# Performance work log

Measured on AMD Instinct MI355X. Metric: run time of the kernel, lower is better.

Reference implementation:

```python
import jax, jax.numpy as jnp
import numpy as np

NUM_HEADS = 16
HEAD_DIM = 64
HIDDEN = NUM_HEADS * HEAD_DIM  # 1024
SEQ_LEN = 4096


def setup_inputs() -> dict:
    key = jax.random.key(0)
    ks = jax.random.split(key, 8)
    hidden_states = jax.random.normal(ks[0], (SEQ_LEN, HIDDEN), dtype=jnp.float32)
    cu_seqlens = jnp.sort(jax.random.randint(ks[1], (5,), 0, SEQ_LEN)).astype(jnp.int32)
    cos = jax.random.uniform(ks[2], (SEQ_LEN, HEAD_DIM), dtype=jnp.float32)
    sin = jax.random.uniform(ks[3], (SEQ_LEN, HEAD_DIM), dtype=jnp.float32)
    W_qkv = jax.random.normal(ks[4], (HIDDEN, 3 * HIDDEN), dtype=jnp.float32) * 0.02
    b_qkv = jax.random.normal(ks[5], (3 * HIDDEN,), dtype=jnp.float32) * 0.02
    W_proj = jax.random.normal(ks[6], (HIDDEN, HIDDEN), dtype=jnp.float32) * 0.02
    b_proj = jax.random.normal(ks[7], (HIDDEN,), dtype=jnp.float32) * 0.02
    return {
        "hidden_states": hidden_states,
        "cu_seqlens": cu_seqlens,
        "cos": cos,
        "sin": sin,
        "W_qkv": W_qkv,
        "b_qkv": b_qkv,
        "W_proj": W_proj,
        "b_proj": b_proj,
    }


def _rotate_half(x):
    x1, x2 = jnp.split(x, 2, axis=-1)
    return jnp.concatenate([-x2, x1], axis=-1)


def reference(hidden_states, cu_seqlens, cos, sin, W_qkv, b_qkv, W_proj, b_proj):
    # NOTE: original module does not use cu_seqlens for masking (full dense attention).
    seq_len = hidden_states.shape[0]
    qkv = hidden_states @ W_qkv + b_qkv  # (S, 3*H)
    qkv = qkv.reshape(seq_len, 3, NUM_HEADS, HEAD_DIM)
    q, k, v = qkv[:, 0], qkv[:, 1], qkv[:, 2]  # (S, nh, hd)
    c = cos[:, None, :]
    s = sin[:, None, :]
    q = q * c + _rotate_half(q) * s
    k = k * c + _rotate_half(k) * s
    scale = 1.0 / jnp.sqrt(jnp.float32(HEAD_DIM))
    # (nh, S, hd)
    q = q.transpose(1, 0, 2)
    k = k.transpose(1, 0, 2)
    v = v.transpose(1, 0, 2)
    attn = jnp.einsum('hqd,hkd->hqk', q, k) * scale
    attn = jax.nn.softmax(attn, axis=-1)
    out = jnp.einsum('hqk,hkd->hqd', attn, v)
    out = out.transpose(1, 0, 2).reshape(seq_len, HIDDEN)
    return out @ W_proj + b_proj
```

## Files before the change

### kernel.cpp

```cpp
#include <hip/hip_runtime.h>
#include <type_traits>

typedef short bf16x8 __attribute__((ext_vector_type(8)));
typedef float f32x4  __attribute__((ext_vector_type(4)));
typedef unsigned short u16;

#define MFMA(a,b,c) __builtin_amdgcn_mfma_f32_16x16x32_bf16((a),(b),(c),0,0,0)

__device__ __forceinline__ float bf2f(u16 u){ unsigned x=((unsigned)u)<<16; return __builtin_bit_cast(float,x); }
__device__ __forceinline__ u16 f2bf(float f){ unsigned x=__builtin_bit_cast(unsigned,f); x += 0x7fffu + ((x>>16)&1u); return (u16)(x>>16); }

#if __has_builtin(__builtin_amdgcn_cvt_pk_bf16_f32)
typedef __bf16 hwbf2 __attribute__((ext_vector_type(2)));
__device__ __forceinline__ unsigned pkbf(float a, float b){
  hwbf2 r = __builtin_amdgcn_cvt_pk_bf16_f32(a, b);
  return __builtin_bit_cast(unsigned, r);
}
#else
__device__ __forceinline__ unsigned pkbf(float a, float b){
  unsigned ua = __builtin_bit_cast(unsigned, a), ub = __builtin_bit_cast(unsigned, b);
  ua += 0x7fffu + ((ua>>16)&1u);
  ub += 0x7fffu + ((ub>>16)&1u);
  return __builtin_amdgcn_perm(ub, ua, 0x07060302u);
}
#endif

#if __has_builtin(__builtin_amdgcn_exp2f)
#define EXP2(x) __builtin_amdgcn_exp2f(x)
#else
#define EXP2(x) exp2f(x)
#endif

__device__ __forceinline__ void async_cp16(const u16* g, u16* l){
  __builtin_amdgcn_global_load_lds((const __attribute__((address_space(1))) void*)g,
                                   (__attribute__((address_space(3))) void*)l, 16, 0, 0);
}

__global__ __launch_bounds__(256) void prep(
    const float* __restrict__ H, const float* __restrict__ Wqkv, const float* __restrict__ Wproj,
    u16* __restrict__ Hb, u16* __restrict__ WqkvT, u16* __restrict__ WprojT)
{
  __shared__ u16 tile[32][33];
  const int bid = blockIdx.x, tid = threadIdx.x;
  if (bid < 4096) {
    int i = (bid*256 + tid)*4;
    float4 v = *(const float4*)(H + i);
    ushort4 o;
    o.x = f2bf(v.x); o.y = f2bf(v.y); o.z = f2bf(v.z); o.w = f2bf(v.w);
    *(ushort4*)(Hb + i) = o;
    return;
  }
  const float* in; u16* out; int R, C, bx, by;
  if (bid < 7168) { int t = bid-4096; in=Wqkv; out=WqkvT; R=1024; C=3072; bx=t%96; by=t/96; }
  else            { int t = bid-7168; in=Wproj; out=WprojT; R=1024; C=1024; bx=t%32; by=t/32; }
  int bc = bx*32, br = by*32;
  int tx = tid & 31, ty = tid >> 5;
  #pragma unroll
  for (int i=ty;i<32;i+=8) tile[i][tx] = f2bf(in[(size_t)(br+i)*C + bc + tx]);
  __syncthreads();
  #pragma unroll
  for (int i=ty;i<32;i+=8) out[(size_t)(bc+i)*R + br + tx] = tile[tx][i];
}

__global__ __launch_bounds__(256) void gemm_qkv_rope(
    const u16* __restrict__ A, const u16* __restrict__ Bt,
    const float* __restrict__ bias, const float* __restrict__ cosb, const float* __restrict__ sinb,
    u16* __restrict__ Qo, u16* __restrict__ Ko, u16* __restrict__ Vo)
{
  constexpr int K = 1024;
  __shared__ __align__(16) u16 As[128*64];
  __shared__ __align__(16) u16 Bs[128*64];
  const int m0 = blockIdx.y*128, n0 = blockIdx.x*128;
  const int tid = threadIdx.x, wave = tid>>6, lane = tid&63;
  const int wr = (wave>>1)*64, wc = (wave&1)*64;
  const int ml = lane&15, quad = lane>>4;
  const int lrow8 = lane>>3, lchk = lane&7;
  const int swzg = (lchk ^ lrow8)*8;
  const u16* gA[4]; u16* lA[4];
  const u16* gB[4]; u16* lB[4];
  #pragma unroll
  for (int t=0;t<4;t++){
    gA[t] = A  + (size_t)(m0 + wave*32 + t*8 + lrow8)*K + swzg;
    lA[t] = &As[(wave*32 + t*8)*64];
    gB[t] = Bt + (size_t)(n0 + wave*32 + t*8 + lrow8)*K + swzg;
    lB[t] = &Bs[(wave*32 + t*8)*64];
  }
  f32x4 acc[4][4] = {};
  const int rch0 = ( quad     ^ (ml&7))*8;
  const int rch1 = ((quad|4) ^ (ml&7))*8;
  for (int k0=0; k0<K; k0+=64) {
    #pragma unroll
    for (int t=0;t<4;t++){ async_cp16(gA[t]+k0, lA[t]); async_cp16(gB[t]+k0, lB[t]); }
    __syncthreads();
    #pragma unroll
    for (int kk=0;kk<2;kk++){
      const int rc = kk ? rch1 : rch0;
      bf16x8 af[4], bfr[4];
      #pragma unroll
      for (int i=0;i<4;i++)  af[i]  = *(const bf16x8*)&As[(wr+i*16+ml)*64 + rc];
      #pragma unroll
      for (int j=0;j<4;j++) bfr[j] = *(const bf16x8*)&Bs[(wc+j*16+ml)*64 + rc];
      #pragma unroll
      for (int i=0;i<4;i++)
        #pragma unroll
        for (int j=0;j<4;j++)
          acc[i][j] = MFMA(af[i], bfr[j], acc[i][j]);
    }
    __syncthreads();
  }
  const int region = n0 >> 10;
  if (region == 2) {
    #pragma unroll
    for (int j=0;j<4;j++){
      int col = n0 + wc + j*16 + ml;
      int dloc = col & 63, hh = (col & 1023) >> 6;
      float bv = bias[col];
      #pragma unroll
      for (int i=0;i<4;i++){
        int row0 = m0 + wr + i*16 + quad*4;
        #pragma unroll
        for (int r=0;r<4;r++)
          Vo[((size_t)hh*4096 + row0 + r)*64 + dloc] = f2bf(acc[i][j][r] + bv);
      }
    }
  } else {
    u16* dst = region ? Ko : Qo;
    const float qs = region ? 1.0f : 0.125f*1.44269504f;
    #pragma unroll
    for (int j=0;j<4;j++){
      int col = n0 + wc + j*16 + ml;
      int dloc = col & 63, hh = (col & 1023) >> 6;
      float bv  = bias[col];
      float bvp = bias[col ^ 32];
      float sgn = (dloc < 32) ? -1.f : 1.f;
      #pragma unroll
      for (int i=0;i<4;i++){
        int row0 = m0 + wr + i*16 + quad*4;
        #pragma unroll
        for (int r=0;r<4;r++){
          int t = row0 + r;
          float c = cosb[t*64 + dloc], s = sinb[t*64 + dloc];
          float val = acc[i][j][r]   + bv;
          float par = acc[i][j^2][r] + bvp;
          dst[((size_t)hh*4096 + t)*64 + dloc] = f2bf((val*c + sgn*par*s)*qs);
        }
      }
    }
  }
}

__global__ __launch_bounds__(256) void vtrans_perm_bf16(const u16* __restrict__ in, u16* __restrict__ out){
  __shared__ u16 tile[32][33];
  const int h = blockIdx.z;
  const u16* ip = in + (size_t)h*4096*64;
  u16* op = out + (size_t)h*64*4096;
  int bt = blockIdx.x*32, bd = blockIdx.y*32;
  int tx = threadIdx.x & 31, ty = threadIdx.x >> 5;
  #pragma unroll
  for (int i=ty;i<32;i+=8) tile[i][tx] = ip[(size_t)(bt+i)*64 + bd + tx];
  __syncthreads();
  const int tlog = ((tx>>2)&1)*16 + (tx>>3)*4 + (tx&3);
  #pragma unroll
  for (int i=ty;i<32;i+=8) op[(size_t)(bd+i)*4096 + bt + tx] = tile[tlog][i];
}

template<int BN, typename OutT>
__global__ __launch_bounds__(256) void gemm_bt_bias(
    const u16* __restrict__ A, const u16* __restrict__ Bt,
    const float* __restrict__ bias, OutT* __restrict__ C,
    int M, int N, int K)
{
  __shared__ __align__(16) u16 As[128*64];
  __shared__ __align__(16) u16 Bs[BN*64];
  const int m0 = blockIdx.y*128, n0 = blockIdx.x*BN;
  const int tid = threadIdx.x, wave = tid>>6, lane = tid&63;
  const int wr = (wave>>1)*64, wc = (wave&1)*(BN/2);
  const int ml = lane&15, quad = lane>>4;
  const int lrow8 = lane>>3, lchk = lane&7;
  const int swzg = (lchk ^ lrow8)*8;
  const u16* gA[4]; u16* lA[4];
  #pragma unroll
  for (int t=0;t<4;t++){
    gA[t] = A + (size_t)(m0 + wave*32 + t*8 + lrow8)*K + swzg;
    lA[t] = &As[(wave*32 + t*8)*64];
  }
  constexpr int BI = BN/32;
  const u16* gB[BI]; u16* lB[BI];
  #pragma unroll
  for (int t=0;t<BI;t++){
    gB[t] = Bt + (size_t)(n0 + wave*(BN/4) + t*8 + lrow8)*K + swzg;
    lB[t] = &Bs[(wave*(BN/4) + t*8)*64];
  }
  constexpr int NJ = BN/32;
  f32x4 acc[4][NJ] = {};
  const int rch0 = ( quad     ^ (ml&7))*8;
  const int rch1 = ((quad|4) ^ (ml&7))*8;
  for (int k0=0; k0<K; k0+=64) {
    #pragma unroll
    for (int t=0;t<4;t++)  async_cp16(gA[t]+k0, lA[t]);
    #pragma unroll
    for (int t=0;t<BI;t++) async_cp16(gB[t]+k0, lB[t]);
    __syncthreads();
    #pragma unroll
    for (int kk=0;kk<2;kk++){
      const int rc = kk ? rch1 : rch0;
      bf16x8 af[4], bfr[NJ];
      #pragma unroll
      for (int i=0;i<4;i++)  af[i]  = *(const bf16x8*)&As[(wr+i*16+ml)*64 + rc];
      #pragma unroll
      for (int j=0;j<NJ;j++) bfr[j] = *(const bf16x8*)&Bs[(wc+j*16+ml)*64 + rc];
      #pragma unroll
      for (int i=0;i<4;i++)
        #pragma unroll
        for (int j=0;j<NJ;j++)
          acc[i][j] = MFMA(af[i], bfr[j], acc[i][j]);
    }
    __syncthreads();
  }
  #pragma unroll
  for (int j=0;j<NJ;j++){
    int col = n0 + wc + j*16 + ml;
    float bv = bias[col];
    #pragma unroll
    for (int i=0;i<4;i++){
      int row0 = m0 + wr + i*16 + quad*4;
      #pragma unroll
      for (int r=0;r<4;r++){
        float val = acc[i][j][r] + bv;
        if constexpr (std::is_same_v<OutT, float>)
          C[(size_t)(row0+r)*N + col] = val;
        else
          C[(size_t)(row0+r)*N + col] = f2bf(val);
      }
    }
  }
}

__global__ __launch_bounds__(256,4) void flash_attn(
    const u16* __restrict__ Q, const u16* __restrict__ Kg, const u16* __restrict__ VT,
    u16* __restrict__ O0, u16* __restrict__ O1, u16* __restrict__ O2, u16* __restrict__ O3,
    float* __restrict__ Lpart)
{
  constexpr int SEQ=4096, QTR=1024;
  __shared__ __align__(16) u16 Ks[64*64];
  __shared__ __align__(16) u16 Vs[64*64];
  const int qt=blockIdx.x, h=blockIdx.y, ks=blockIdx.z;
  const int tid=threadIdx.x, wave=tid>>6, lane=tid&63;
  const int ml=lane&15, quad=lane>>4;
  const int qbase = qt*128 + wave*32;
  bf16x8 qf[2][2];
  #pragma unroll
  for (int qi=0; qi<2; qi++){
    const u16* qp = Q + ((size_t)h*SEQ + qbase + qi*16 + ml)*64;
    qf[qi][0] = *(const bf16x8*)(qp + quad*8);
    qf[qi][1] = *(const bf16x8*)(qp + 32 + quad*8);
  }
  const bf16x8 ones = {0x3F80,0x3F80,0x3F80,0x3F80,0x3F80,0x3F80,0x3F80,0x3F80};
  f32x4 o[2][4] = {};
  f32x4 accsum[2] = {};
  const int lrow8 = lane>>3, lchk = lane&7;
  const int swzg = (lchk ^ lrow8)*8;
  const u16* kgl = Kg + (size_t)h*SEQ*64 + (size_t)(ks*QTR + wave*16 + lrow8)*64 + swzg;
  const u16* vgl = VT + (size_t)h*64*SEQ + (size_t)(wave*16 + lrow8)*SEQ + ks*QTR + swzg;
  u16* kl0 = &Ks[(wave*16  )*64];
  u16* kl1 = &Ks[(wave*16+8)*64];
  u16* vl0 = &Vs[(wave*16  )*64];
  u16* vl1 = &Vs[(wave*16+8)*64];
  const int swzA = ( quad     ^ (ml&7))*8;
  const int swzB = ((quad^4) ^ (ml&7))*8;

  for (int k0=0;k0<QTR;k0+=64) {
    async_cp16(kgl + (size_t)k0*64,       kl0);
    async_cp16(kgl + (size_t)k0*64 + 512, kl1);
    async_cp16(vgl + k0,                  vl0);
    async_cp16(vgl + 8*SEQ + k0,          vl1);
    __syncthreads();
    f32x4 s[2][4];
    #pragma unroll
    for (int kb=0;kb<4;kb++){
      bf16x8 kf0 = *(const bf16x8*)&Ks[(kb*16+ml)*64 + swzA];
      bf16x8 kf1 = *(const bf16x8*)&Ks[(kb*16+ml)*64 + swzB];
      f32x4 z0={0,0,0,0}, z1={0,0,0,0};
      z0 = MFMA(kf0, qf[0][0], z0); s[0][kb] = MFMA(kf1, qf[0][1], z0);
      z1 = MFMA(kf0, qf[1][0], z1); s[1][kb] = MFMA(kf1, qf[1][1], z1);
    }
    bf16x8 vf[4][2];
    #pragma unroll
    for (int db=0;db<4;db++){
      vf[db][0] = *(const bf16x8*)&Vs[(db*16+ml)*64 + swzA];
      vf[db][1] = *(const bf16x8*)&Vs[(db*16+ml)*64 + swzB];
    }
    #pragma unroll
    for (int qi=0; qi<2; qi++)
      #pragma unroll
      for (int p=0;p<2;p++){
        float e0 = EXP2(s[qi][2*p][0]),   e1 = EXP2(s[qi][2*p][1]);
        float e2 = EXP2(s[qi][2*p][2]),   e3 = EXP2(s[qi][2*p][3]);
        float e4 = EXP2(s[qi][2*p+1][0]), e5 = EXP2(s[qi][2*p+1][1]);
        float e6 = EXP2(s[qi][2*p+1][2]), e7 = EXP2(s[qi][2*p+1][3]);
        union { uint4 u; bf16x8 v; } pf;
        pf.u.x = pkbf(e0,e1); pf.u.y = pkbf(e2,e3);
        pf.u.z = pkbf(e4,e5); pf.u.w = pkbf(e6,e7);
        accsum[qi] = MFMA(ones, pf.v, accsum[qi]);
        #pragma unroll
        for (int db=0;db<4;db++)
          o[qi][db] = MFMA(vf[db][p], pf.v, o[qi][db]);
      }
    __syncthreads();
  }
  u16* op = (ks==0) ? O0 : (ks==1) ? O1 : (ks==2) ? O2 : O3;
  #pragma unroll
  for (int qi=0;qi<2;qi++){
    size_t rb = (size_t)(qbase + qi*16 + ml)*1024 + h*64;
    #pragma unroll
    for (int db=0;db<4;db++){
      uint2 w;
      w.x = pkbf(o[qi][db][0], o[qi][db][1]);
      w.y = pkbf(o[qi][db][2], o[qi][db][3]);
      *(uint2*)&op[rb + db*16 + quad*4] = w;
    }
  }
  if (quad==0){
    float* lp = Lpart + (size_t)ks*65536 + (size_t)h*4096 + qbase;
    lp[ml]    = accsum[0][0];
    lp[16+ml] = accsum[1][0];
  }
}

__global__ __launch_bounds__(256) void combine_softmax4(
    const u16* __restrict__ O0, const u16* __restrict__ O1,
    const u16* __restrict__ O2, const u16* __restrict__ O3,
    const float* __restrict__ L, u16* __restrict__ AO)
{
  int i = (blockIdx.x*256 + threadIdx.x)*4;
  int row = i >> 10, col = i & 1023, h = col >> 6;
  int li = h*4096 + row;
  float inv = 1.f/(L[li] + L[li+65536] + L[li+2*65536] + L[li+3*65536]);
  ushort4 a = *(const ushort4*)(O0+i);
  ushort4 b = *(const ushort4*)(O1+i);
  ushort4 c = *(const ushort4*)(O2+i);
  ushort4 d = *(const ushort4*)(O3+i);
  ushort4 o;
  o.x = f2bf((bf2f(a.x)+bf2f(b.x)+bf2f(c.x)+bf2f(d.x))*inv);
  o.y = f2bf((bf2f(a.y)+bf2f(b.y)+bf2f(c.y)+bf2f(d.y))*inv);
  o.z = f2bf((bf2f(a.z)+bf2f(b.z)+bf2f(c.z)+bf2f(d.z))*inv);
  o.w = f2bf((bf2f(a.w)+bf2f(b.w)+bf2f(c.w)+bf2f(d.w))*inv);
  *(ushort4*)(AO+i) = o;
}

extern "C" void kernel_launch(void* const* d_in, const int* in_sizes, int n_in,
                              void* d_out, int out_size, void* d_ws, size_t ws_size,
                              hipStream_t stream)
{
  (void)in_sizes; (void)n_in; (void)out_size; (void)ws_size;
  const float* H     = (const float*)d_in[0];
  const float* cosb  = (const float*)d_in[2];
  const float* sinb  = (const float*)d_in[3];
  const float* Wqkv  = (const float*)d_in[4];
  const float* bqkv  = (const float*)d_in[5];
  const float* Wproj = (const float*)d_in[6];
  const float* bproj = (const float*)d_in[7];
  float* out = (float*)d_out;
  char* ws = (char*)d_ws;
  float* Lpart  = (float*)(ws + 0);
  u16*   WprojT = (u16*)(ws + 2097152);
  u16*   Hb     = (u16*)(ws + 4194304);
  u16*   VTb    = (u16*)(ws + 4194304);
  u16*   Qb     = (u16*)(ws + 12582912);
  u16*   AO     = (u16*)(ws + 12582912);
  u16*   Kb     = (u16*)(ws + 20971520);
  u16*   Vb     = (u16*)(ws + 29360128);
  u16*   Opart3 = (u16*)(ws + 29360128);
  u16*   WqkvT  = (u16*)(ws + 37748736);
  u16*   Opart0 = (u16*)(ws + 37748736);
  u16*   Opart1 = (u16*)(ws + 46137344);
  u16*   Opart2 = (u16*)(ws + 54525952);

  hipLaunchKernelGGL(prep, dim3(8192), dim3(256), 0, stream, H, Wqkv, Wproj, Hb, WqkvT, WprojT);
  hipLaunchKernelGGL(gemm_qkv_rope, dim3(24,32), dim3(256), 0, stream,
                     Hb, WqkvT, bqkv, cosb, sinb, Qb, Kb, Vb);
  hipLaunchKernelGGL(vtrans_perm_bf16, dim3(128,2,16), dim3(256), 0, stream, Vb, VTb);
  hipLaunchKernelGGL(flash_attn, dim3(32,16,4), dim3(256), 0, stream, Qb, Kb, VTb,
                     Opart0, Opart1, Opart2, Opart3, Lpart);
  hipLaunchKernelGGL(combine_softmax4, dim3(4096), dim3(256), 0, stream,
                     Opart0, Opart1, Opart2, Opart3, Lpart, AO);
  hipLaunchKernelGGL((gemm_bt_bias<64,float>), dim3(16,32), dim3(256), 0, stream,
                     AO, WprojT, bproj, out, 4096, 1024, 1024);
}
```

Measured before the change: 246.6 us.

## Double-buffer K/V tiles in LDS to overlap loads with attention compute

```diff
diff --git a/kernel.cpp b/kernel.cpp
--- a/kernel.cpp
+++ b/kernel.cpp
@@ -241,9 +241,9 @@
     u16* __restrict__ O0, u16* __restrict__ O1, u16* __restrict__ O2, u16* __restrict__ O3,
     float* __restrict__ Lpart)
 {
-  constexpr int SEQ=4096, QTR=1024;
-  __shared__ __align__(16) u16 Ks[64*64];
-  __shared__ __align__(16) u16 Vs[64*64];
+  constexpr int SEQ=4096, QTR=1024, NT=QTR/64;
+  __shared__ __align__(16) u16 Ks[2][64*64];
+  __shared__ __align__(16) u16 Vs[2][64*64];
   const int qt=blockIdx.x, h=blockIdx.y, ks=blockIdx.z;
   const int tid=threadIdx.x, wave=tid>>6, lane=tid&63;
   const int ml=lane&15, quad=lane>>4;
@@ -262,24 +262,24 @@
   const int swzg = (lchk ^ lrow8)*8;
   const u16* kgl = Kg + (size_t)h*SEQ*64 + (size_t)(ks*QTR + wave*16 + lrow8)*64 + swzg;
   const u16* vgl = VT + (size_t)h*64*SEQ + (size_t)(wave*16 + lrow8)*SEQ + ks*QTR + swzg;
-  u16* kl0 = &Ks[(wave*16  )*64];
-  u16* kl1 = &Ks[(wave*16+8)*64];
-  u16* vl0 = &Vs[(wave*16  )*64];
-  u16* vl1 = &Vs[(wave*16+8)*64];
   const int swzA = ( quad     ^ (ml&7))*8;
   const int swzB = ((quad^4) ^ (ml&7))*8;
 
-  for (int k0=0;k0<QTR;k0+=64) {
-    async_cp16(kgl + (size_t)k0*64,       kl0);
-    async_cp16(kgl + (size_t)k0*64 + 512, kl1);
-    async_cp16(vgl + k0,                  vl0);
-    async_cp16(vgl + 8*SEQ + k0,          vl1);
-    __syncthreads();
+  auto stage = [&](int k0, int b){
+    u16* kb_ = (u16*)&Ks[b][0];
+    u16* vb_ = (u16*)&Vs[b][0];
+    async_cp16(kgl + (size_t)k0*64,       kb_ + (wave*16  )*64);
+    async_cp16(kgl + (size_t)k0*64 + 512, kb_ + (wave*16+8)*64);
+    async_cp16(vgl + k0,                  vb_ + (wave*16  )*64);
+    async_cp16(vgl + 8*SEQ + k0,          vb_ + (wave*16+8)*64);
+  };
+
+  auto compute_tile = [&](const u16* Kc, const u16* Vc){
     f32x4 s[2][4];
     #pragma unroll
     for (int kb=0;kb<4;kb++){
-      bf16x8 kf0 = *(const bf16x8*)&Ks[(kb*16+ml)*64 + swzA];
-      bf16x8 kf1 = *(const bf16x8*)&Ks[(kb*16+ml)*64 + swzB];
+      bf16x8 kf0 = *(const bf16x8*)&Kc[(kb*16+ml)*64 + swzA];
+      bf16x8 kf1 = *(const bf16x8*)&Kc[(kb*16+ml)*64 + swzB];
       f32x4 z0={0,0,0,0}, z1={0,0,0,0};
       z0 = MFMA(kf0, qf[0][0], z0); s[0][kb] = MFMA(kf1, qf[0][1], z0);
       z1 = MFMA(kf0, qf[1][0], z1); s[1][kb] = MFMA(kf1, qf[1][1], z1);
@@ -287,8 +287,8 @@
     bf16x8 vf[4][2];
     #pragma unroll
     for (int db=0;db<4;db++){
-      vf[db][0] = *(const bf16x8*)&Vs[(db*16+ml)*64 + swzA];
-      vf[db][1] = *(const bf16x8*)&Vs[(db*16+ml)*64 + swzB];
+      vf[db][0] = *(const bf16x8*)&Vc[(db*16+ml)*64 + swzA];
+      vf[db][1] = *(const bf16x8*)&Vc[(db*16+ml)*64 + swzB];
     }
     #pragma unroll
     for (int qi=0; qi<2; qi++)
@@ -306,8 +306,23 @@
         for (int db=0;db<4;db++)
           o[qi][db] = MFMA(vf[db][p], pf.v, o[qi][db]);
       }
-    __syncthreads();
-  }
+  };
+
+  const u16* Ks0 = &Ks[0][0]; const u16* Vs0 = &Vs[0][0];
+  const u16* Ks1 = &Ks[1][0]; const u16* Vs1 = &Vs[1][0];
+
+  stage(0, 0);
+  __syncthreads();
+  #pragma unroll 1
+  for (int it=0; it<NT; it+=2){
+    if (it+1 < NT) stage((it+1)*64, 1);
+    compute_tile(Ks0, Vs0);
+    __syncthreads();
+    if (it+2 < NT) stage((it+2)*64, 0);
+    compute_tile(Ks1, Vs1);
+    __syncthreads();
+  }
+
   u16* op = (ks==0) ? O0 : (ks==1) ? O1 : (ks==2) ? O2 : O3;
   #pragma unroll
   for (int qi=0;qi<2;qi++){
```

Result: slower. 309.5 us (+25.5%).
